# Kernel optimization log

Measured on AMD Instinct MI355X. Metric: run time of the kernel, lower is better.

## Reference

```python
import jax, jax.numpy as jnp
import numpy as np

NA, NB, NG, D = 250000, 500000, 50000, 64
EA, EG = 1000000, 500000


def setup_inputs() -> dict:
    key = jax.random.key(0)
    k = jax.random.split(key, 7)
    return {
        "atom_ft": jax.random.normal(k[0], (NA, D), dtype=jnp.float32),
        "bond_ft": jax.random.normal(k[1], (NB, D), dtype=jnp.float32),
        "global_ft": jax.random.normal(k[2], (NG, D), dtype=jnp.float32),
        "a2b_src": jax.random.randint(k[3], (EA,), 0, NA, dtype=jnp.int32),
        "a2b_dst": jax.random.randint(k[4], (EA,), 0, NB, dtype=jnp.int32),
        "g2b_src": jax.random.randint(k[5], (EG,), 0, NG, dtype=jnp.int32),
        "g2b_dst": jax.random.randint(k[6], (EG,), 0, NB, dtype=jnp.int32),
    }


def _mean_max(src_ft, src, dst, n_dst):
    # copy_u: gather source-node features onto edges, then segment-reduce to dst
    m = src_ft[src]  # [E, D]
    s = jax.ops.segment_sum(m, dst, num_segments=n_dst)  # [n_dst, D]
    cnt = jax.ops.segment_sum(jnp.ones((dst.shape[0], 1), src_ft.dtype), dst,
                              num_segments=n_dst)  # [n_dst, 1]
    mean = s / jnp.maximum(cnt, 1.0)
    mx = jax.ops.segment_max(m, dst, num_segments=n_dst)
    # DGL fills zero-in-degree nodes with 0 for both mean and max
    mx = jnp.where(cnt > 0, mx, 0.0)
    return mean, mx


def reference(atom_ft, bond_ft, global_ft, a2b_src, a2b_dst, g2b_src, g2b_dst):
    nb = bond_ft.shape[0]
    # etype ('atom','a2b','bond')
    mean_a, max_a = _mean_max(atom_ft, a2b_src, a2b_dst, nb)
    ft = jnp.concatenate([bond_ft, mean_a, max_a], axis=1)  # [NB, 3D]
    # etype ('global','g2b','bond') — applied to the widened bond features
    mean_g, max_g = _mean_max(global_ft, g2b_src, g2b_dst, nb)
    ft = jnp.concatenate([ft, mean_g, max_g], axis=1)  # [NB, 5D]
    return (atom_ft, ft, global_ft)
```

## Files before the change

kernel.cpp:

```cpp
#include <hip/hip_runtime.h>

#define NA 250000
#define NB 500000
#define NG 50000
#define DD 64
#define EA_N 1000000
#define EG_N 500000
#define FTC 320
#define NSEG (2 * NB)
#define SCAN_BLK 1024
#define NSCAN_BLKS ((NSEG + SCAN_BLK - 1) / SCAN_BLK)

#define BOND_BLKS (NB / 16)
#define COPYA_BLKS 1024
#define COPYG_BLKS 128

typedef float vf4 __attribute__((ext_vector_type(4)));


__device__ __forceinline__ float4 f4add(float4 a, float4 b) {
    return make_float4(a.x + b.x, a.y + b.y, a.z + b.z, a.w + b.w);
}
__device__ __forceinline__ float4 f4max(float4 a, float4 b) {
    return make_float4(fmaxf(a.x, b.x), fmaxf(a.y, b.y),
                       fmaxf(a.z, b.z), fmaxf(a.w, b.w));
}
__device__ __forceinline__ float4 f4scale(float4 a, float s) {
    return make_float4(a.x * s, a.y * s, a.z * s, a.w * s);
}
__device__ __forceinline__ float4 ntload4(const float4* p) {
    vf4 v = __builtin_nontemporal_load((const vf4*)p);
    return make_float4(v.x, v.y, v.z, v.w);
}
__device__ __forceinline__ void ntstore4(float4 a, float4* p) {
    vf4 v = {a.x, a.y, a.z, a.w};
    __builtin_nontemporal_store(v, (vf4*)p);
}


__global__ void count_kernel(const int4* __restrict__ a2b_dst4,
                             const int4* __restrict__ g2b_dst4,
                             int* __restrict__ cnt) {
    int i = blockIdx.x * blockDim.x + threadIdx.x;
    int stride = gridDim.x * blockDim.x;
    const int totalA = EA_N / 4;
    const int total = (EA_N + EG_N) / 4;
    for (; i < total; i += stride) {
        if (i < totalA) {
            int4 d = a2b_dst4[i];
            atomicAdd(&cnt[d.x], 1);
            atomicAdd(&cnt[d.y], 1);
            atomicAdd(&cnt[d.z], 1);
            atomicAdd(&cnt[d.w], 1);
        } else {
            int4 d = g2b_dst4[i - totalA];
            atomicAdd(&cnt[NB + d.x], 1);
            atomicAdd(&cnt[NB + d.y], 1);
            atomicAdd(&cnt[NB + d.z], 1);
            atomicAdd(&cnt[NB + d.w], 1);
        }
    }
}

__global__ void scan1_kernel(const int* __restrict__ cnt,
                             int* __restrict__ offs,
                             int* __restrict__ bsum) {
    __shared__ int sm[SCAN_BLK];
    int tid = threadIdx.x;
    int idx = blockIdx.x * SCAN_BLK + tid;
    int v = (idx < NSEG) ? cnt[idx] : 0;
    sm[tid] = v;
    __syncthreads();
    for (int off = 1; off < SCAN_BLK; off <<= 1) {
        int t = (tid >= off) ? sm[tid - off] : 0;
        __syncthreads();
        sm[tid] += t;
        __syncthreads();
    }
    if (idx < NSEG) offs[idx] = sm[tid] - v;
    if (tid == SCAN_BLK - 1) bsum[blockIdx.x] = sm[tid];
}

__global__ void scan2_kernel(int* __restrict__ bsum) {
    __shared__ int sm[SCAN_BLK];
    int tid = threadIdx.x;
    int v = (tid < NSCAN_BLKS) ? bsum[tid] : 0;
    sm[tid] = v;
    __syncthreads();
    for (int off = 1; off < SCAN_BLK; off <<= 1) {
        int t = (tid >= off) ? sm[tid - off] : 0;
        __syncthreads();
        sm[tid] += t;
        __syncthreads();
    }
    if (tid < NSCAN_BLKS) bsum[tid] = sm[tid] - v;
}

__global__ void scan3_kernel(int* __restrict__ offs,
                             const int* __restrict__ bsum,
                             int* __restrict__ cursor) {
    int idx = blockIdx.x * SCAN_BLK + threadIdx.x;
    if (idx < NSEG) {
        int o = offs[idx] + bsum[blockIdx.x];
        offs[idx] = o;
        cursor[idx] = o;
    }
    if (idx == 0) offs[NSEG] = EA_N + EG_N;
}

__global__ void fill_kernel(const int4* __restrict__ a2b_src4,
                            const int4* __restrict__ a2b_dst4,
                            const int4* __restrict__ g2b_src4,
                            const int4* __restrict__ g2b_dst4,
                            int* __restrict__ cursor,
                            int* __restrict__ esrc) {
    int i = blockIdx.x * blockDim.x + threadIdx.x;
    int stride = gridDim.x * blockDim.x;
    const int totalA = EA_N / 4;
    const int total = (EA_N + EG_N) / 4;
    for (; i < total; i += stride) {
        int4 d, s;
        int base;
        if (i < totalA) {
            d = a2b_dst4[i]; s = a2b_src4[i]; base = 0;
        } else {
            d = g2b_dst4[i - totalA]; s = g2b_src4[i - totalA]; base = NB;
        }
        int p0 = atomicAdd(&cursor[base + d.x], 1); esrc[p0] = s.x;
        int p1 = atomicAdd(&cursor[base + d.y], 1); esrc[p1] = s.y;
        int p2 = atomicAdd(&cursor[base + d.z], 1); esrc[p2] = s.z;
        int p3 = atomicAdd(&cursor[base + d.w], 1); esrc[p3] = s.w;
    }
}


__global__ __launch_bounds__(256) void mega_kernel(
    const float4* __restrict__ bond4, const float4* __restrict__ atom4,
    const float4* __restrict__ glob4, const int* __restrict__ offs,
    const int* __restrict__ esrc, float4* __restrict__ ft4,
    float4* __restrict__ out_atom4, float4* __restrict__ out_glob4) {
    int bid = blockIdx.x;

    if (bid < BOND_BLKS) {
        long long b = (long long)bid * 16 + (threadIdx.x >> 4);
        int q = threadIdx.x & 15;
        int gbase = threadIdx.x & 48;

        int a0 = offs[b], a1 = offs[b + 1];
        int g0 = offs[NB + b], g1 = offs[NB + b + 1];
        float4 bv = ntload4(&bond4[b * 16 + q]);

        int dega = a1 - a0;
        int degg = g1 - g0;

        int my_sa = (q < dega) ? esrc[a0 + q] : 0;
        int my_sg = (q < degg) ? esrc[g0 + q] : 0;

        float4 sa = make_float4(0.f, 0.f, 0.f, 0.f);
        float4 xa = make_float4(-INFINITY, -INFINITY, -INFINITY, -INFINITY);
        int na = min(dega, 16);
        for (int j = 0; j < na; ++j) {
            int s = __shfl(my_sa, gbase + j, 64);
            float4 v = atom4[(long long)s * 16 + q];
            sa = f4add(sa, v);
            xa = f4max(xa, v);
        }
        for (int e = a0 + 16; e < a1; ++e) {
            int s = esrc[e];
            float4 v = atom4[(long long)s * 16 + q];
            sa = f4add(sa, v);
            xa = f4max(xa, v);
        }

        float4 sg = make_float4(0.f, 0.f, 0.f, 0.f);
        float4 xg = make_float4(-INFINITY, -INFINITY, -INFINITY, -INFINITY);
        int ng = min(degg, 16);
        for (int j = 0; j < ng; ++j) {
            int s = __shfl(my_sg, gbase + j, 64);
            float4 v = glob4[(long long)s * 16 + q];
            sg = f4add(sg, v);
            xg = f4max(xg, v);
        }
        for (int e = g0 + 16; e < g1; ++e) {
            int s = esrc[e];
            float4 v = glob4[(long long)s * 16 + q];
            sg = f4add(sg, v);
            xg = f4max(xg, v);
        }

        float4 ma = f4scale(sa, dega ? 1.f / (float)dega : 0.f);
        if (!dega) xa = make_float4(0.f, 0.f, 0.f, 0.f);
        float4 mg = f4scale(sg, degg ? 1.f / (float)degg : 0.f);
        if (!degg) xg = make_float4(0.f, 0.f, 0.f, 0.f);

        float4* row = ft4 + b * 80;
        ntstore4(bv, &row[q]);
        ntstore4(ma, &row[16 + q]);
        ntstore4(xa, &row[32 + q]);
        ntstore4(mg, &row[48 + q]);
        ntstore4(xg, &row[64 + q]);
    } else if (bid < BOND_BLKS + COPYA_BLKS) {
        long long n4 = (long long)NA * DD / 4;
        long long i = (long long)(bid - BOND_BLKS) * 256 + threadIdx.x;
        long long stride = (long long)COPYA_BLKS * 256;
        for (; i < n4; i += stride) {
            float4 v = ntload4(&atom4[i]);
            ntstore4(v, &out_atom4[i]);
        }
    } else {
        long long n4 = (long long)NG * DD / 4;
        long long i = (long long)(bid - BOND_BLKS - COPYA_BLKS) * 256 + threadIdx.x;
        long long stride = (long long)COPYG_BLKS * 256;
        for (; i < n4; i += stride) {
            float4 v = ntload4(&glob4[i]);
            ntstore4(v, &out_glob4[i]);
        }
    }
}


extern "C" void kernel_launch(void* const* d_in, const int* in_sizes, int n_in,
                              void* d_out, int out_size, void* d_ws, size_t ws_size,
                              hipStream_t stream) {
    const float* atom_ft   = (const float*)d_in[0];
    const float* bond_ft   = (const float*)d_in[1];
    const float* global_ft = (const float*)d_in[2];
    const int* a2b_src = (const int*)d_in[3];
    const int* a2b_dst = (const int*)d_in[4];
    const int* g2b_src = (const int*)d_in[5];
    const int* g2b_dst = (const int*)d_in[6];

    float* out = (float*)d_out;
    float* out_atom = out;
    float* out_ft   = out + (long long)NA * DD;
    float* out_glob = out_ft + (long long)NB * FTC;

    int* ws      = (int*)d_ws;
    int* cnt     = ws;
    int* offs    = ws + 1000000;
    int* cursor  = ws + 2000004;
    int* bsum    = ws + 3000004;
    int* esrc    = ws + 3001028;

    const int BLK = 256;

    (void)hipMemsetAsync(cnt, 0, (size_t)NSEG * sizeof(int), stream);

    const int EDGE4_BLKS = ((EA_N + EG_N) / 4 + BLK - 1) / BLK;
    count_kernel<<<EDGE4_BLKS, BLK, 0, stream>>>(
        (const int4*)a2b_dst, (const int4*)g2b_dst, cnt);

    scan1_kernel<<<NSCAN_BLKS, SCAN_BLK, 0, stream>>>(cnt, offs, bsum);
    scan2_kernel<<<1, SCAN_BLK, 0, stream>>>(bsum);
    scan3_kernel<<<NSCAN_BLKS, SCAN_BLK, 0, stream>>>(offs, bsum, cursor);

    fill_kernel<<<EDGE4_BLKS, BLK, 0, stream>>>(
        (const int4*)a2b_src, (const int4*)a2b_dst,
        (const int4*)g2b_src, (const int4*)g2b_dst, cursor, esrc);

    mega_kernel<<<BOND_BLKS + COPYA_BLKS + COPYG_BLKS, BLK, 0, stream>>>(
        (const float4*)bond_ft, (const float4*)atom_ft,
        (const float4*)global_ft, offs, esrc, (float4*)out_ft,
        (float4*)out_atom, (float4*)out_glob);
}
```

Measured before the change: 390.7 us.

## Overlap feature copies with counting, merge scans, process two bonds per thread

The atom and global feature copies move out of the final gather kernel and into the edge-count kernel, so the bandwidth-bound copy runs alongside the atomic-bound counting. The scan2 and scan3 kernels merge into one kernel in which each block reduces the preceding block sums itself, removing a launch. The bond kernel now handles two bonds per 16-lane group and interleaves their four gather streams to raise memory-level parallelism. Index loads and esrc stores use nontemporal hints. In exchange there are more registers per thread and half as many blocks in the bond kernel, and each scan block repeats the block-sum reduction.

```diff
diff --git a/kernel.cpp b/kernel.cpp
--- a/kernel.cpp
+++ b/kernel.cpp
@@ -11,11 +11,13 @@
 #define SCAN_BLK 1024
 #define NSCAN_BLKS ((NSEG + SCAN_BLK - 1) / SCAN_BLK)
 
-#define BOND_BLKS (NB / 16)
+#define EDGE4_BLKS (((EA_N + EG_N) / 4 + 255) / 256)
 #define COPYA_BLKS 1024
 #define COPYG_BLKS 128
+#define BOND_BLKS (NB / 32)
 
 typedef float vf4 __attribute__((ext_vector_type(4)));
+typedef int   vi4 __attribute__((ext_vector_type(4)));
 
 
 __device__ __forceinline__ float4 f4add(float4 a, float4 b) {
@@ -36,31 +38,56 @@
     vf4 v = {a.x, a.y, a.z, a.w};
     __builtin_nontemporal_store(v, (vf4*)p);
 }
-
-
-__global__ void count_kernel(const int4* __restrict__ a2b_dst4,
-                             const int4* __restrict__ g2b_dst4,
-                             int* __restrict__ cnt) {
-    int i = blockIdx.x * blockDim.x + threadIdx.x;
-    int stride = gridDim.x * blockDim.x;
-    const int totalA = EA_N / 4;
-    const int total = (EA_N + EG_N) / 4;
-    for (; i < total; i += stride) {
-        if (i < totalA) {
-            int4 d = a2b_dst4[i];
-            atomicAdd(&cnt[d.x], 1);
-            atomicAdd(&cnt[d.y], 1);
-            atomicAdd(&cnt[d.z], 1);
-            atomicAdd(&cnt[d.w], 1);
-        } else {
-            int4 d = g2b_dst4[i - totalA];
-            atomicAdd(&cnt[NB + d.x], 1);
-            atomicAdd(&cnt[NB + d.y], 1);
-            atomicAdd(&cnt[NB + d.z], 1);
-            atomicAdd(&cnt[NB + d.w], 1);
-        }
-    }
-}
+__device__ __forceinline__ vi4 ntload_i4(const int* p) {
+    return __builtin_nontemporal_load((const vi4*)p);
+}
+
+
+__global__ __launch_bounds__(256) void count_copy_kernel(
+    const int* __restrict__ a2b_dst, const int* __restrict__ g2b_dst,
+    int* __restrict__ cnt,
+    const float4* __restrict__ atom4, float4* __restrict__ out_atom4,
+    const float4* __restrict__ glob4, float4* __restrict__ out_glob4) {
+    int bid = blockIdx.x;
+    if (bid < EDGE4_BLKS) {
+        int i = bid * blockDim.x + threadIdx.x;
+        int stride = EDGE4_BLKS * blockDim.x;
+        const int totalA = EA_N / 4;
+        const int total = (EA_N + EG_N) / 4;
+        for (; i < total; i += stride) {
+            if (i < totalA) {
+                vi4 d = ntload_i4(a2b_dst + 4 * i);
+                atomicAdd(&cnt[d.x], 1);
+                atomicAdd(&cnt[d.y], 1);
+                atomicAdd(&cnt[d.z], 1);
+                atomicAdd(&cnt[d.w], 1);
+            } else {
+                vi4 d = ntload_i4(g2b_dst + 4 * (i - totalA));
+                atomicAdd(&cnt[NB + d.x], 1);
+                atomicAdd(&cnt[NB + d.y], 1);
+                atomicAdd(&cnt[NB + d.z], 1);
+                atomicAdd(&cnt[NB + d.w], 1);
+            }
+        }
+    } else if (bid < EDGE4_BLKS + COPYA_BLKS) {
+        long long n4 = (long long)NA * DD / 4;
+        long long i = (long long)(bid - EDGE4_BLKS) * 256 + threadIdx.x;
+        long long stride = (long long)COPYA_BLKS * 256;
+        for (; i < n4; i += stride) {
+            float4 v = ntload4(&atom4[i]);
+            ntstore4(v, &out_atom4[i]);
+        }
+    } else {
+        long long n4 = (long long)NG * DD / 4;
+        long long i = (long long)(bid - EDGE4_BLKS - COPYA_BLKS) * 256 + threadIdx.x;
+        long long stride = (long long)COPYG_BLKS * 256;
+        for (; i < n4; i += stride) {
+            float4 v = ntload4(&glob4[i]);
+            ntstore4(v, &out_glob4[i]);
+        }
+    }
+}
+
 
 __global__ void scan1_kernel(const int* __restrict__ cnt,
                              int* __restrict__ offs,
@@ -81,37 +108,33 @@
     if (tid == SCAN_BLK - 1) bsum[blockIdx.x] = sm[tid];
 }
 
-__global__ void scan2_kernel(int* __restrict__ bsum) {
-    __shared__ int sm[SCAN_BLK];
+__global__ void scan23_kernel(int* __restrict__ offs,
+                              const int* __restrict__ bsum,
+                              int* __restrict__ cursor) {
+    __shared__ int red[SCAN_BLK];
     int tid = threadIdx.x;
-    int v = (tid < NSCAN_BLKS) ? bsum[tid] : 0;
-    sm[tid] = v;
+    int bid = blockIdx.x;
+    red[tid] = (tid < bid) ? bsum[tid] : 0;
     __syncthreads();
-    for (int off = 1; off < SCAN_BLK; off <<= 1) {
-        int t = (tid >= off) ? sm[tid - off] : 0;
+    for (int off = SCAN_BLK / 2; off > 0; off >>= 1) {
+        if (tid < off) red[tid] += red[tid + off];
         __syncthreads();
-        sm[tid] += t;
-        __syncthreads();
-    }
-    if (tid < NSCAN_BLKS) bsum[tid] = sm[tid] - v;
-}
-
-__global__ void scan3_kernel(int* __restrict__ offs,
-                             const int* __restrict__ bsum,
-                             int* __restrict__ cursor) {
-    int idx = blockIdx.x * SCAN_BLK + threadIdx.x;
+    }
+    int base = red[0];
+    int idx = bid * SCAN_BLK + tid;
     if (idx < NSEG) {
-        int o = offs[idx] + bsum[blockIdx.x];
+        int o = offs[idx] + base;
         offs[idx] = o;
         cursor[idx] = o;
     }
-    if (idx == 0) offs[NSEG] = EA_N + EG_N;
-}
-
-__global__ void fill_kernel(const int4* __restrict__ a2b_src4,
-                            const int4* __restrict__ a2b_dst4,
-                            const int4* __restrict__ g2b_src4,
-                            const int4* __restrict__ g2b_dst4,
+    if (bid == 0 && tid == 0) offs[NSEG] = EA_N + EG_N;
+}
+
+
+__global__ void fill_kernel(const int* __restrict__ a2b_src,
+                            const int* __restrict__ a2b_dst,
+                            const int* __restrict__ g2b_src,
+                            const int* __restrict__ g2b_dst,
                             int* __restrict__ cursor,
                             int* __restrict__ esrc) {
     int i = blockIdx.x * blockDim.x + threadIdx.x;
@@ -119,103 +142,124 @@
     const int totalA = EA_N / 4;
     const int total = (EA_N + EG_N) / 4;
     for (; i < total; i += stride) {
-        int4 d, s;
+        vi4 d, s;
         int base;
         if (i < totalA) {
-            d = a2b_dst4[i]; s = a2b_src4[i]; base = 0;
+            d = ntload_i4(a2b_dst + 4 * i);
+            s = ntload_i4(a2b_src + 4 * i);
+            base = 0;
         } else {
-            d = g2b_dst4[i - totalA]; s = g2b_src4[i - totalA]; base = NB;
-        }
-        int p0 = atomicAdd(&cursor[base + d.x], 1); esrc[p0] = s.x;
-        int p1 = atomicAdd(&cursor[base + d.y], 1); esrc[p1] = s.y;
-        int p2 = atomicAdd(&cursor[base + d.z], 1); esrc[p2] = s.z;
-        int p3 = atomicAdd(&cursor[base + d.w], 1); esrc[p3] = s.w;
-    }
-}
-
-
-__global__ __launch_bounds__(256) void mega_kernel(
+            d = ntload_i4(g2b_dst + 4 * (i - totalA));
+            s = ntload_i4(g2b_src + 4 * (i - totalA));
+            base = NB;
+        }
+        int p0 = atomicAdd(&cursor[base + d.x], 1);
+        int p1 = atomicAdd(&cursor[base + d.y], 1);
+        int p2 = atomicAdd(&cursor[base + d.z], 1);
+        int p3 = atomicAdd(&cursor[base + d.w], 1);
+        __builtin_nontemporal_store(s.x, &esrc[p0]);
+        __builtin_nontemporal_store(s.y, &esrc[p1]);
+        __builtin_nontemporal_store(s.z, &esrc[p2]);
+        __builtin_nontemporal_store(s.w, &esrc[p3]);
+    }
+}
+
+
+__global__ __launch_bounds__(256) void bond_kernel(
     const float4* __restrict__ bond4, const float4* __restrict__ atom4,
     const float4* __restrict__ glob4, const int* __restrict__ offs,
-    const int* __restrict__ esrc, float4* __restrict__ ft4,
-    float4* __restrict__ out_atom4, float4* __restrict__ out_glob4) {
-    int bid = blockIdx.x;
-
-    if (bid < BOND_BLKS) {
-        long long b = (long long)bid * 16 + (threadIdx.x >> 4);
-        int q = threadIdx.x & 15;
-        int gbase = threadIdx.x & 48;
-
-        int a0 = offs[b], a1 = offs[b + 1];
-        int g0 = offs[NB + b], g1 = offs[NB + b + 1];
-        float4 bv = ntload4(&bond4[b * 16 + q]);
-
-        int dega = a1 - a0;
-        int degg = g1 - g0;
-
-        int my_sa = (q < dega) ? esrc[a0 + q] : 0;
-        int my_sg = (q < degg) ? esrc[g0 + q] : 0;
-
-        float4 sa = make_float4(0.f, 0.f, 0.f, 0.f);
-        float4 xa = make_float4(-INFINITY, -INFINITY, -INFINITY, -INFINITY);
-        int na = min(dega, 16);
-        for (int j = 0; j < na; ++j) {
-            int s = __shfl(my_sa, gbase + j, 64);
+    const int* __restrict__ esrc, float4* __restrict__ ft4) {
+    long long b0 = (long long)blockIdx.x * 32 + (threadIdx.x >> 4);
+    long long b1 = b0 + 16;
+    int q = threadIdx.x & 15;
+    int gbase = threadIdx.x & 48;
+
+    int a00 = offs[b0], a01 = offs[b0 + 1];
+    int g00 = offs[NB + b0], g01 = offs[NB + b0 + 1];
+    int a10 = offs[b1], a11 = offs[b1 + 1];
+    int g10 = offs[NB + b1], g11 = offs[NB + b1 + 1];
+    float4 bv0 = ntload4(&bond4[b0 * 16 + q]);
+    float4 bv1 = ntload4(&bond4[b1 * 16 + q]);
+
+    int da0 = a01 - a00, dg0 = g01 - g00;
+    int da1 = a11 - a10, dg1 = g11 - g10;
+
+    int ia0 = (q < da0) ? esrc[a00 + q] : 0;
+    int ig0 = (q < dg0) ? esrc[g00 + q] : 0;
+    int ia1 = (q < da1) ? esrc[a10 + q] : 0;
+    int ig1 = (q < dg1) ? esrc[g10 + q] : 0;
+
+    float4 sa0 = make_float4(0.f, 0.f, 0.f, 0.f), sa1 = sa0, sg0 = sa0, sg1 = sa0;
+    float4 xa0 = make_float4(-INFINITY, -INFINITY, -INFINITY, -INFINITY);
+    float4 xa1 = xa0, xg0 = xa0, xg1 = xa0;
+
+    int na0 = min(da0, 16), na1 = min(da1, 16);
+    int ng0 = min(dg0, 16), ng1 = min(dg1, 16);
+    int nmax = max(max(na0, na1), max(ng0, ng1));
+    for (int j = 0; j < nmax; ++j) {
+        if (j < na0) {
+            int s = __shfl(ia0, gbase + j, 64);
             float4 v = atom4[(long long)s * 16 + q];
-            sa = f4add(sa, v);
-            xa = f4max(xa, v);
-        }
-        for (int e = a0 + 16; e < a1; ++e) {
-            int s = esrc[e];
+            sa0 = f4add(sa0, v); xa0 = f4max(xa0, v);
+        }
+        if (j < na1) {
+            int s = __shfl(ia1, gbase + j, 64);
             float4 v = atom4[(long long)s * 16 + q];
-            sa = f4add(sa, v);
-            xa = f4max(xa, v);
-        }
-
-        float4 sg = make_float4(0.f, 0.f, 0.f, 0.f);
-        float4 xg = make_float4(-INFINITY, -INFINITY, -INFINITY, -INFINITY);
-        int ng = min(degg, 16);
-        for (int j = 0; j < ng; ++j) {
-            int s = __shfl(my_sg, gbase + j, 64);
+            sa1 = f4add(sa1, v); xa1 = f4max(xa1, v);
+        }
+        if (j < ng0) {
+            int s = __shfl(ig0, gbase + j, 64);
             float4 v = glob4[(long long)s * 16 + q];
-            sg = f4add(sg, v);
-            xg = f4max(xg, v);
-        }
-        for (int e = g0 + 16; e < g1; ++e) {
-            int s = esrc[e];
+            sg0 = f4add(sg0, v); xg0 = f4max(xg0, v);
+        }
+        if (j < ng1) {
+            int s = __shfl(ig1, gbase + j, 64);
             float4 v = glob4[(long long)s * 16 + q];
-            sg = f4add(sg, v);
-            xg = f4max(xg, v);
-        }
-
-        float4 ma = f4scale(sa, dega ? 1.f / (float)dega : 0.f);
-        if (!dega) xa = make_float4(0.f, 0.f, 0.f, 0.f);
-        float4 mg = f4scale(sg, degg ? 1.f / (float)degg : 0.f);
-        if (!degg) xg = make_float4(0.f, 0.f, 0.f, 0.f);
-
-        float4* row = ft4 + b * 80;
-        ntstore4(bv, &row[q]);
-        ntstore4(ma, &row[16 + q]);
-        ntstore4(xa, &row[32 + q]);
-        ntstore4(mg, &row[48 + q]);
-        ntstore4(xg, &row[64 + q]);
-    } else if (bid < BOND_BLKS + COPYA_BLKS) {
-        long long n4 = (long long)NA * DD / 4;
-        long long i = (long long)(bid - BOND_BLKS) * 256 + threadIdx.x;
-        long long stride = (long long)COPYA_BLKS * 256;
-        for (; i < n4; i += stride) {
-            float4 v = ntload4(&atom4[i]);
-            ntstore4(v, &out_atom4[i]);
-        }
-    } else {
-        long long n4 = (long long)NG * DD / 4;
-        long long i = (long long)(bid - BOND_BLKS - COPYA_BLKS) * 256 + threadIdx.x;
-        long long stride = (long long)COPYG_BLKS * 256;
-        for (; i < n4; i += stride) {
-            float4 v = ntload4(&glob4[i]);
-            ntstore4(v, &out_glob4[i]);
-        }
-    }
+            sg1 = f4add(sg1, v); xg1 = f4max(xg1, v);
+        }
+    }
+    for (int e = a00 + 16; e < a01; ++e) {
+        int s = esrc[e];
+        float4 v = atom4[(long long)s * 16 + q];
+        sa0 = f4add(sa0, v); xa0 = f4max(xa0, v);
+    }
+    for (int e = a10 + 16; e < a11; ++e) {
+        int s = esrc[e];
+        float4 v = atom4[(long long)s * 16 + q];
+        sa1 = f4add(sa1, v); xa1 = f4max(xa1, v);
+    }
+    for (int e = g00 + 16; e < g01; ++e) {
+        int s = esrc[e];
+        float4 v = glob4[(long long)s * 16 + q];
+        sg0 = f4add(sg0, v); xg0 = f4max(xg0, v);
+    }
+    for (int e = g10 + 16; e < g11; ++e) {
+        int s = esrc[e];
+        float4 v = glob4[(long long)s * 16 + q];
+        sg1 = f4add(sg1, v); xg1 = f4max(xg1, v);
+    }
+
+    float4 ma0 = f4scale(sa0, da0 ? 1.f / (float)da0 : 0.f);
+    float4 ma1 = f4scale(sa1, da1 ? 1.f / (float)da1 : 0.f);
+    float4 mg0 = f4scale(sg0, dg0 ? 1.f / (float)dg0 : 0.f);
+    float4 mg1 = f4scale(sg1, dg1 ? 1.f / (float)dg1 : 0.f);
+    if (!da0) xa0 = make_float4(0.f, 0.f, 0.f, 0.f);
+    if (!da1) xa1 = make_float4(0.f, 0.f, 0.f, 0.f);
+    if (!dg0) xg0 = make_float4(0.f, 0.f, 0.f, 0.f);
+    if (!dg1) xg1 = make_float4(0.f, 0.f, 0.f, 0.f);
+
+    float4* row0 = ft4 + b0 * 80;
+    ntstore4(bv0, &row0[q]);
+    ntstore4(ma0, &row0[16 + q]);
+    ntstore4(xa0, &row0[32 + q]);
+    ntstore4(mg0, &row0[48 + q]);
+    ntstore4(xg0, &row0[64 + q]);
+    float4* row1 = ft4 + b1 * 80;
+    ntstore4(bv1, &row1[q]);
+    ntstore4(ma1, &row1[16 + q]);
+    ntstore4(xa1, &row1[32 + q]);
+    ntstore4(mg1, &row1[48 + q]);
+    ntstore4(xg1, &row1[64 + q]);
 }
 
 
@@ -246,20 +290,18 @@
 
     (void)hipMemsetAsync(cnt, 0, (size_t)NSEG * sizeof(int), stream);
 
-    const int EDGE4_BLKS = ((EA_N + EG_N) / 4 + BLK - 1) / BLK;
-    count_kernel<<<EDGE4_BLKS, BLK, 0, stream>>>(
-        (const int4*)a2b_dst, (const int4*)g2b_dst, cnt);
+    count_copy_kernel<<<EDGE4_BLKS + COPYA_BLKS + COPYG_BLKS, BLK, 0, stream>>>(
+        a2b_dst, g2b_dst, cnt,
+        (const float4*)atom_ft, (float4*)out_atom,
+        (const float4*)global_ft, (float4*)out_glob);
 
     scan1_kernel<<<NSCAN_BLKS, SCAN_BLK, 0, stream>>>(cnt, offs, bsum);
-    scan2_kernel<<<1, SCAN_BLK, 0, stream>>>(bsum);
-    scan3_kernel<<<NSCAN_BLKS, SCAN_BLK, 0, stream>>>(offs, bsum, cursor);
+    scan23_kernel<<<NSCAN_BLKS, SCAN_BLK, 0, stream>>>(offs, bsum, cursor);
 
     fill_kernel<<<EDGE4_BLKS, BLK, 0, stream>>>(
-        (const int4*)a2b_src, (const int4*)a2b_dst,
-        (const int4*)g2b_src, (const int4*)g2b_dst, cursor, esrc);
-
-    mega_kernel<<<BOND_BLKS + COPYA_BLKS + COPYG_BLKS, BLK, 0, stream>>>(
+        a2b_src, a2b_dst, g2b_src, g2b_dst, cursor, esrc);
+
+    bond_kernel<<<BOND_BLKS, BLK, 0, stream>>>(
         (const float4*)bond_ft, (const float4*)atom_ft,
-        (const float4*)global_ft, offs, esrc, (float4*)out_ft,
-        (float4*)out_atom, (float4*)out_glob);
-}
+        (const float4*)global_ft, offs, esrc, (float4*)out_ft);
+}
```

After: 415.0 us. 6.2% more time.
